# Optimization experiments

Measured on AMD Instinct MI355X. Metric: run time of the kernel, lower is better.

The kernel has to match this reference:

```python
import jax, jax.numpy as jnp
import numpy as np
from jax import lax

S, B, I, H, L = 512, 64, 256, 1024, 2

def setup_inputs() -> dict:
    key = jax.random.key(0)
    ks = jax.random.split(key, 9)
    s = 1.0 / np.sqrt(H)
    return {
        "x": jax.random.normal(ks[0], (S, B, I), jnp.float32),
        "W_in": jax.random.normal(ks[1], (H, I), jnp.float32) * (1.0 / np.sqrt(I)),
        "b_in": jax.random.normal(ks[2], (H,), jnp.float32) * 0.01,
        "W_ih": jax.random.normal(ks[3], (L, H, H), jnp.float32) * s,
        "W_hh": jax.random.normal(ks[4], (L, H, H), jnp.float32) * s,
        "b_ih": jax.random.normal(ks[5], (L, H), jnp.float32) * 0.01,
        "b_hh": jax.random.normal(ks[6], (L, H), jnp.float32) * 0.01,
        "W_out": jax.random.normal(ks[7], (I, H), jnp.float32) * s,
        "b_out": jax.random.normal(ks[8], (I,), jnp.float32) * 0.01,
    }

def reference(x, W_in, b_in, W_ih, W_hh, b_ih, b_hh, W_out, b_out):
    # in_layer: [S,B,I] -> [S,B,H]
    inp = jnp.einsum('sbi,hi->sbh', x, W_in) + b_in
    h0 = jnp.zeros((B, H), dtype=x.dtype)  # hidden=None -> zeros
    h_finals = []
    for l in range(L):  # fixed small layer loop
        # input-to-hidden GEMM batched over all timesteps
        pre = jnp.einsum('sbh,gh->sbg', inp, W_ih[l]) + b_ih[l]  # [S,B,H]
        Whh_l, bhh_l = W_hh[l], b_hh[l]
        def step(h, p, Whh=Whh_l, bhh=bhh_l):
            h_new = jnp.tanh(p + h @ Whh.T + bhh)
            return h_new, h_new
        h_last, inp = lax.scan(step, h0, pre)
        h_finals.append(h_last)
    hidden = jnp.stack(h_finals)  # [L,B,H]
    output = jnp.einsum('sbh,ih->sbi', inp, W_out) + b_out  # [S,B,I]
    return output, hidden
```

## Files before the change

kernel.cpp:

```cpp
#include <hip/hip_runtime.h>
#include <stdint.h>

#define SEQ 512
#define BAT 64
#define INF 256
#define HID 1024
#define SB  (SEQ*BAT)
#define G_WGS 64
#define NWG (3*G_WGS)

typedef __attribute__((ext_vector_type(8))) short short8;
typedef __attribute__((ext_vector_type(4))) float f32x4;

union Frag8 { uint32_t u[4]; short8 s; };

__device__ __forceinline__ uint32_t bf16hi_rne(uint32_t u){
  return (u + 0x7FFFu + ((u >> 16) & 1u)) & 0xFFFF0000u;
}
__device__ __forceinline__ uint32_t pack_split(float v){
  uint32_t hi = bf16hi_rne(__float_as_uint(v));
  float r = v - __uint_as_float(hi);
  uint32_t lo = bf16hi_rne(__float_as_uint(r)) >> 16;
  return hi | lo;
}
__device__ __forceinline__ void unpack_pair(uint32_t u0, uint32_t u1,
                                            uint32_t& h, uint32_t& l){
  h = __builtin_amdgcn_perm(u1, u0, 0x07060302u);
  l = __builtin_amdgcn_perm(u1, u0, 0x05040100u);
}
__device__ __forceinline__ void gl16(const void* g, void* l){
  __builtin_amdgcn_global_load_lds(
      (const __attribute__((address_space(1))) void*)g,
      (__attribute__((address_space(3))) void*)l, 16, 0, 0);
}

__device__ __forceinline__ void astore32(uint32_t* p, uint32_t v){
  __hip_atomic_store(p, v, __ATOMIC_RELAXED, __HIP_MEMORY_SCOPE_AGENT);
}
__device__ __forceinline__ void waitflags32(const uint32_t* base, uint32_t tgt){
  const int lane = threadIdx.x & 63;
  unsigned spins = 0;
  for (;;){
    uint32_t v = (lane < 32)
        ? __hip_atomic_load(base + lane, __ATOMIC_RELAXED, __HIP_MEMORY_SCOPE_AGENT)
        : 0xFFFFFFFFu;
    if (__all(v >= tgt)) break;
    __builtin_amdgcn_s_sleep(1);
    if (++spins > (1u << 20)) break;
  }
}

__global__ __launch_bounds__(256) void wcomb_kernel(const float* __restrict__ A,
                                                    const float* __restrict__ B,
                                                    float* __restrict__ C){
  __shared__ float As[16][64];
  __shared__ float Bs[64][256];
  const int tid = threadIdx.x;
  const int g0 = blockIdx.x * 16;
  float acc[16];
#pragma unroll
  for (int g = 0; g < 16; ++g) acc[g] = 0.f;
  for (int h0 = 0; h0 < HID; h0 += 64){
    __syncthreads();
#pragma unroll
    for (int j = 0; j < 4; ++j){
      int c = j*256 + tid;
      As[c >> 6][c & 63] = A[(size_t)(g0 + (c >> 6))*HID + h0 + (c & 63)];
    }
#pragma unroll
    for (int j = 0; j < 64; ++j) Bs[j][tid] = B[(size_t)(h0 + j)*INF + tid];
    __syncthreads();
#pragma unroll
    for (int hh = 0; hh < 64; hh += 4){
      float b0 = Bs[hh][tid], b1 = Bs[hh+1][tid], b2 = Bs[hh+2][tid], b3 = Bs[hh+3][tid];
#pragma unroll
      for (int g = 0; g < 16; ++g){
        const float4 a = *(const float4*)&As[g][hh];
        acc[g] += a.x*b0 + a.y*b1 + a.z*b2 + a.w*b3;
      }
    }
  }
#pragma unroll
  for (int g = 0; g < 16; ++g) C[(size_t)(g0 + g)*INF + tid] = acc[g];
}

__global__ __launch_bounds__(256) void bcomb_kernel(const float* __restrict__ Wih0,
                                                    const float* __restrict__ bin,
                                                    const float* __restrict__ bih0,
                                                    float* __restrict__ bcomb){
  __shared__ float r[4];
  const int g = blockIdx.x, tid = threadIdx.x;
  float s = 0.f;
  for (int h = tid; h < HID; h += 256) s += Wih0[(size_t)g*HID + h] * bin[h];
  for (int o = 32; o > 0; o >>= 1) s += __shfl_down(s, o, 64);
  if ((tid & 63) == 0) r[tid >> 6] = s;
  __syncthreads();
  if (tid == 0) bcomb[g] = bih0[g] + r[0] + r[1] + r[2] + r[3];
}

__global__ void split_w(const float* __restrict__ in, uint16_t* __restrict__ hi,
                        uint16_t* __restrict__ lo, int n){
  int i = blockIdx.x*256 + threadIdx.x;
  if (i < n){
    float v = in[i];
    uint32_t h = bf16hi_rne(__float_as_uint(v));
    float r = v - __uint_as_float(h);
    hi[i] = (uint16_t)(h >> 16);
    lo[i] = (uint16_t)(bf16hi_rne(__float_as_uint(r)) >> 16);
  }
}

__global__ void pack_x(const float* __restrict__ in, uint32_t* __restrict__ out, int n){
  int i = blockIdx.x*256 + threadIdx.x;
  if (i < n) out[i] = pack_split(in[i]);
}

__global__ __launch_bounds__(256) void gemm_split(
    const uint32_t* __restrict__ A, const uint16_t* __restrict__ Whi,
    const uint16_t* __restrict__ Wlo, const float* __restrict__ bias,
    float* __restrict__ C, int N, int K)
{
  __shared__ uint32_t Al[128*32];
  __shared__ uint16_t Wh[128*32];
  __shared__ uint16_t Wl[128*32];
  const int tid  = threadIdx.x;
  const int lane = tid & 63;
  const int w    = tid >> 6;
  const int wm   = w >> 1, wn = w & 1;
  const int lr   = lane & 15, kg = lane >> 4;
  const int bm   = blockIdx.x, bn = blockIdx.y;

  const uint32_t* Ag  = A   + (size_t)bm*128*K;
  const uint16_t* Whg = Whi + (size_t)bn*128*K;
  const uint16_t* Wlg = Wlo + (size_t)bn*128*K;

  f32x4 acc[4][4];
#pragma unroll
  for (int i = 0; i < 4; ++i)
#pragma unroll
    for (int j = 0; j < 4; ++j) acc[i][j] = (f32x4){0.f,0.f,0.f,0.f};

  for (int ks = 0; ks < K; ks += 32){
    __syncthreads();
#pragma unroll
    for (int j = 0; j < 4; ++j){
      int c = j*256 + tid;
      int row = c >> 3, kc = c & 7;
      int kcs = kc ^ ((row & 3) << 1);
      gl16(Ag + (size_t)row*K + ks + kcs*4, (char*)Al + c*16);
    }
#pragma unroll
    for (int j = 0; j < 2; ++j){
      int c = j*256 + tid;
      int row = c >> 2, kc = c & 3;
      int kcs = kc ^ (row & 3);
      gl16(Whg + (size_t)row*K + ks + kcs*8, (char*)Wh + c*16);
      gl16(Wlg + (size_t)row*K + ks + kcs*8, (char*)Wl + c*16);
    }
    __syncthreads();

    short8 ah[4], al[4];
#pragma unroll
    for (int mt = 0; mt < 4; ++mt){
      int row = wm*64 + mt*16 + lr;
      int c2  = kg ^ (row & 3);
      const uint32_t* p = &Al[row*32 + c2*8];
      uint4 a0 = *(const uint4*)p;
      uint4 a1 = *(const uint4*)(p + 4);
      Frag8 fh, fl;
      unpack_pair(a0.x, a0.y, fh.u[0], fl.u[0]);
      unpack_pair(a0.z, a0.w, fh.u[1], fl.u[1]);
      unpack_pair(a1.x, a1.y, fh.u[2], fl.u[2]);
      unpack_pair(a1.z, a1.w, fh.u[3], fl.u[3]);
      ah[mt] = fh.s; al[mt] = fl.s;
    }
#pragma unroll
    for (int nt = 0; nt < 4; ++nt){
      int row = wn*64 + nt*16 + lr;
      int kc  = kg ^ (row & 3);
      short8 whf = *(const short8*)&Wh[row*32 + kc*8];
      short8 wlf = *(const short8*)&Wl[row*32 + kc*8];
#pragma unroll
      for (int mt = 0; mt < 4; ++mt){
        acc[mt][nt] = __builtin_amdgcn_mfma_f32_16x16x32_bf16(ah[mt], whf, acc[mt][nt], 0,0,0);
        acc[mt][nt] = __builtin_amdgcn_mfma_f32_16x16x32_bf16(al[mt], whf, acc[mt][nt], 0,0,0);
        acc[mt][nt] = __builtin_amdgcn_mfma_f32_16x16x32_bf16(ah[mt], wlf, acc[mt][nt], 0,0,0);
      }
    }
  }
#pragma unroll
  for (int nt = 0; nt < 4; ++nt){
    int col = bn*128 + wn*64 + nt*16 + lr;
    float bv = bias[col];
#pragma unroll
    for (int mt = 0; mt < 4; ++mt){
#pragma unroll
      for (int r = 0; r < 4; ++r){
        int rowg = bm*128 + wm*64 + mt*16 + kg*4 + r;
        C[(size_t)rowg*N + col] = acc[mt][nt][r] + bv;
      }
    }
  }
}

__global__ __launch_bounds__(256, 1) void rnn_persist(
    const float* __restrict__ pre0, uint32_t* __restrict__ h0seq,
    uint32_t* __restrict__ pre1, uint32_t* __restrict__ h1seq,
    const uint16_t* __restrict__ Whh0h, const uint16_t* __restrict__ Whh0l,
    const uint16_t* __restrict__ Wih1h, const uint16_t* __restrict__ Wih1l,
    const uint16_t* __restrict__ Whh1h, const uint16_t* __restrict__ Whh1l,
    const float* __restrict__ bhh0, const float* __restrict__ bih1,
    const float* __restrict__ bhh1,
    uint32_t* h0s, uint32_t* h1s,
    uint32_t* ctr, int T, int first)
{
  __shared__ short WhF[32768];
  __shared__ short WlF[32768];
  __shared__ uint32_t Stage[4][2048];
  const int tid  = threadIdx.x;
  const int lane = tid & 63;
  const int w    = tid >> 6;
  const int mt   = w & 1, kh = w >> 1;
  const int lr   = lane & 15, kg = lane >> 4;
  const int wg   = blockIdx.x;
  const int group = wg / G_WGS;
  const int sub  = wg % G_WGS;
  const int rh   = sub >> 5;
  const int ci   = sub & 31;
  const int col0 = ci * 32;

  uint32_t* fmy = ctr + (group*2 + rh)*64;
  uint32_t* f0  = ctr + (0*2 + rh)*64;
  uint32_t* f1  = ctr + (1*2 + rh)*64;
  uint32_t* f2  = ctr + (2*2 + rh)*64;

  const uint16_t* Whg = (group == 0) ? Whh0h : (group == 1) ? Wih1h : Whh1h;
  const uint16_t* Wlg = (group == 0) ? Whh0l : (group == 1) ? Wih1l : Whh1l;

#pragma unroll
  for (int it = 0; it < 16; ++it){
    int lin = it*256 + tid;
    int c = lin >> 7, j = lin & 127;
    int dst = (((c >> 4)*32 + (j >> 2))*64 + (j & 3)*16 + (c & 15))*8;
    *(uint4*)&WhF[dst] = *(const uint4*)&Whg[(size_t)(col0 + c)*HID + j*8];
    *(uint4*)&WlF[dst] = *(const uint4*)&Wlg[(size_t)(col0 + c)*HID + j*8];
  }
  __syncthreads();

  const int p3r = ((lr & 3) << 1) | ((lr >> 2) & 1);
  const int fb0 = 0*16384 + lane*8;
  const int fb1 = 1*16384 + lane*8;
  const int colE = col0 + kh*16 + lr;
  float bvE = 0.f;
  if (group == 0) bvE = bhh0[colE];
  else if (group == 1) bvE = bih1[colE] + bhh1[colE];

  const int R = T + 2;
  for (int r = 0; r < R; ++r){
    const int t = r - group;
    const bool valid = (t >= 0 && t < T);

    if (valid){
      if (group == 0){
        if (t > 0) waitflags32(f0, (uint32_t)t);
      } else if (group == 1){
        waitflags32(f0, (uint32_t)(t+1));
      } else {
        waitflags32(f1, (uint32_t)(t+1));
        if (t > 0) waitflags32(f2, (uint32_t)t);
      }
      asm volatile("" ::: "memory");

      const uint32_t* Ap;
      if (group == 0)
        Ap = (t == 0) ? (first ? (const uint32_t*)0 : h0s)
                      : h0seq + (size_t)(t-1)*(BAT*HID);
      else if (group == 1)
        Ap = h0seq + (size_t)t*(BAT*HID);
      else
        Ap = (t == 0) ? (first ? (const uint32_t*)0 : h1s)
                      : h1seq + (size_t)(t-1)*(BAT*HID);

      const int rowb = rh*32 + mt*16 + kg*4;
      const size_t idxE = (size_t)t*(BAT*HID) + (size_t)rowb*HID + colE;
      float pv[4] = {0,0,0,0};
      if (group == 0){
#pragma unroll
        for (int q = 0; q < 4; ++q) pv[q] = pre0[idxE + (size_t)q*HID];
      } else if (group == 2){
#pragma unroll
        for (int q = 0; q < 4; ++q) pv[q] = __uint_as_float(pre1[idxE + (size_t)q*HID]);
      }

      f32x4 acc[2][2];
#pragma unroll
      for (int i = 0; i < 2; ++i)
#pragma unroll
        for (int j = 0; j < 2; ++j) acc[i][j] = (f32x4){0.f,0.f,0.f,0.f};

      if (Ap){
        const uint32_t* Aw = Ap + (size_t)(rh*32 + mt*16)*HID + kh*512;
        auto STAGE = [&](int c){
          char* dstbase = (char*)&Stage[w][(c & 1)*1024];
#pragma unroll
          for (int j = 0; j < 4; ++j){
            const int slot  = j*64 + lane;
            const int row_l = slot >> 4;
            const int pos   = slot & 15;
            const int p3 = ((row_l & 3) << 1) | ((row_l >> 2) & 1);
            gl16(Aw + (size_t)row_l*HID + c*64 + (pos ^ p3)*4,
                 dstbase + j*1024 + lane*16);
          }
        };

        STAGE(0);
#pragma unroll
        for (int c = 0; c < 8; ++c){
          if (c < 7){
            STAGE(c+1);
            asm volatile("s_waitcnt vmcnt(4)" ::: "memory");
          } else {
            asm volatile("s_waitcnt vmcnt(0)" ::: "memory");
          }
          const uint32_t* Ab = &Stage[w][(c & 1)*1024 + lr*64];
#pragma unroll
          for (int ksl = 0; ksl < 2; ++ksl){
            const int p0 = (ksl*8 + kg*2) ^ p3r;
            uint4 a0 = *(const uint4*)&Ab[p0*4];
            uint4 a1 = *(const uint4*)&Ab[(p0^1)*4];
            Frag8 fh, fl;
            unpack_pair(a0.x, a0.y, fh.u[0], fl.u[0]);
            unpack_pair(a0.z, a0.w, fh.u[1], fl.u[1]);
            unpack_pair(a1.x, a1.y, fh.u[2], fl.u[2]);
            unpack_pair(a1.z, a1.w, fh.u[3], fl.u[3]);
            const int ks = kh*16 + c*2 + ksl;
            short8 wh0 = *(const short8*)&WhF[fb0 + ks*512];
            short8 wl0 = *(const short8*)&WlF[fb0 + ks*512];
            short8 wh1 = *(const short8*)&WhF[fb1 + ks*512];
            short8 wl1 = *(const short8*)&WlF[fb1 + ks*512];
            acc[0][ksl] = __builtin_amdgcn_mfma_f32_16x16x32_bf16(fh.s, wh0, acc[0][ksl], 0,0,0);
            acc[0][ksl] = __builtin_amdgcn_mfma_f32_16x16x32_bf16(fl.s, wh0, acc[0][ksl], 0,0,0);
            acc[0][ksl] = __builtin_amdgcn_mfma_f32_16x16x32_bf16(fh.s, wl0, acc[0][ksl], 0,0,0);
            acc[1][ksl] = __builtin_amdgcn_mfma_f32_16x16x32_bf16(fh.s, wh1, acc[1][ksl], 0,0,0);
            acc[1][ksl] = __builtin_amdgcn_mfma_f32_16x16x32_bf16(fl.s, wh1, acc[1][ksl], 0,0,0);
            acc[1][ksl] = __builtin_amdgcn_mfma_f32_16x16x32_bf16(fh.s, wl1, acc[1][ksl], 0,0,0);
          }
        }
      }
      f32x4 sA = acc[0][0] + acc[0][1];
      f32x4 sB = acc[1][0] + acc[1][1];

      {
        f32x4 give = (kh == 0) ? sB : sA;
        *(f32x4*)&Stage[w][lane*8] = give;
        asm volatile("s_waitcnt lgkmcnt(0)" ::: "memory");
      }
      __builtin_amdgcn_s_barrier();
      {
        const int pw = w ^ 2;
        f32x4 part = *(const f32x4*)&Stage[pw][lane*8];
        f32x4 sE = (kh == 0) ? (sA + part) : (part + sB);

        if (group == 0){
#pragma unroll
          for (int q = 0; q < 4; ++q){
            float v = tanhf(sE[q] + pv[q] + bvE);
            uint32_t pk = pack_split(v);
            astore32(h0seq + idxE + (size_t)q*HID, pk);
            if (t == T-1) astore32(h0s + (size_t)(rowb + q)*HID + colE, pk);
          }
        } else if (group == 1){
#pragma unroll
          for (int q = 0; q < 4; ++q)
            astore32(pre1 + idxE + (size_t)q*HID, __float_as_uint(sE[q] + bvE));
        } else {
#pragma unroll
          for (int q = 0; q < 4; ++q){
            float v = tanhf(sE[q] + pv[q]);
            uint32_t pk = pack_split(v);
            astore32(h1seq + idxE + (size_t)q*HID, pk);
            if (t == T-1) astore32(h1s + (size_t)(rowb + q)*HID + colE, pk);
          }
        }
        asm volatile("s_waitcnt vmcnt(0)" ::: "memory");
      }
      __builtin_amdgcn_s_barrier();
      if (tid == 0)
        astore32(fmy + ci, (uint32_t)(t + 1));
    }
  }
}

__global__ void extract_hidden(const uint32_t* __restrict__ h0s,
                               const uint32_t* __restrict__ h1s,
                               float* __restrict__ out){
  int i = blockIdx.x*256 + threadIdx.x;
  uint32_t p = (i >> 16) ? h1s[i & 65535] : h0s[i & 65535];
  out[(size_t)SB*INF + i] = __uint_as_float(p & 0xFFFF0000u) + __uint_as_float(p << 16);
}

extern "C" void kernel_launch(void* const* d_in, const int* in_sizes, int n_in,
                              void* d_out, int out_size, void* d_ws, size_t ws_size,
                              hipStream_t stream)
{
  const float* x    = (const float*)d_in[0];
  const float* W_in = (const float*)d_in[1];
  const float* b_in = (const float*)d_in[2];
  const float* W_ih = (const float*)d_in[3];
  const float* W_hh = (const float*)d_in[4];
  const float* b_ih = (const float*)d_in[5];
  const float* b_hh = (const float*)d_in[6];
  const float* W_out= (const float*)d_in[7];
  const float* b_out= (const float*)d_in[8];
  float* out = (float*)d_out;
  (void)in_sizes; (void)n_in; (void)out_size;

  const size_t fixedB = 16257024 + 16384;
  const size_t perT   = 1114112;
  int T = 512;
  while (T > 2 && fixedB + (size_t)T*perT + 65536 > ws_size) T >>= 1;
  const int nchunk = SEQ / T;

  char* ws = (char*)d_ws;
  size_t off = 0;
  auto alloc = [&](size_t bytes)->void*{
    void* p = ws + off; off += (bytes + 255) & ~(size_t)255; return p;
  };
  float*    pre0s  = (float*)   alloc((size_t)T*BAT*HID*4);
  uint32_t* h0seq  = (uint32_t*)alloc((size_t)T*BAT*HID*4);
  uint32_t* pre1s  = (uint32_t*)alloc((size_t)T*BAT*HID*4);
  uint32_t* h1seq  = (uint32_t*)alloc((size_t)T*BAT*HID*4);
  uint32_t* xp     = (uint32_t*)alloc((size_t)T*BAT*INF*4);
  float*    WcombF = (float*)   alloc((size_t)HID*INF*4);
  uint16_t* Wc_hi  = (uint16_t*)alloc((size_t)HID*INF*2);
  uint16_t* Wc_lo  = (uint16_t*)alloc((size_t)HID*INF*2);
  uint16_t* Wih1_hi= (uint16_t*)alloc((size_t)HID*HID*2);
  uint16_t* Wih1_lo= (uint16_t*)alloc((size_t)HID*HID*2);
  uint16_t* Whh0_hi= (uint16_t*)alloc((size_t)HID*HID*2);
  uint16_t* Whh0_lo= (uint16_t*)alloc((size_t)HID*HID*2);
  uint16_t* Whh1_hi= (uint16_t*)alloc((size_t)HID*HID*2);
  uint16_t* Whh1_lo= (uint16_t*)alloc((size_t)HID*HID*2);
  uint16_t* Wout_hi= (uint16_t*)alloc((size_t)INF*HID*2);
  uint16_t* Wout_lo= (uint16_t*)alloc((size_t)INF*HID*2);
  float*    bcomb  = (float*)   alloc((size_t)HID*4);
  uint32_t* h0s    = (uint32_t*)alloc((size_t)BAT*HID*4);
  uint32_t* h1s    = (uint32_t*)alloc((size_t)BAT*HID*4);
  uint32_t* ctr    = (uint32_t*)alloc(8192);

  wcomb_kernel<<<HID/16, 256, 0, stream>>>(W_ih, W_in, WcombF);
  bcomb_kernel<<<HID, 256, 0, stream>>>(W_ih, b_in, b_ih, bcomb);
  split_w<<<(HID*INF+255)/256, 256, 0, stream>>>(WcombF, Wc_hi, Wc_lo, HID*INF);
  split_w<<<(HID*HID+255)/256, 256, 0, stream>>>(W_ih + (size_t)HID*HID, Wih1_hi, Wih1_lo, HID*HID);
  split_w<<<(HID*HID+255)/256, 256, 0, stream>>>(W_hh, Whh0_hi, Whh0_lo, HID*HID);
  split_w<<<(HID*HID+255)/256, 256, 0, stream>>>(W_hh + (size_t)HID*HID, Whh1_hi, Whh1_lo, HID*HID);
  split_w<<<(INF*HID+255)/256, 256, 0, stream>>>(W_out, Wout_hi, Wout_lo, INF*HID);

  for (int c = 0; c < nchunk; ++c){
    const float* xc = x + (size_t)c*T*BAT*INF;
    pack_x<<<T*BAT*INF/256, 256, 0, stream>>>(xc, xp, T*BAT*INF);
    gemm_split<<<dim3(T*64/128, HID/128), 256, 0, stream>>>(xp, Wc_hi, Wc_lo, bcomb, pre0s, HID, INF);
    hipMemsetAsync(ctr, 0, 8192, stream);
    rnn_persist<<<NWG, 256, 0, stream>>>(
        pre0s, h0seq, pre1s, h1seq,
        Whh0_hi, Whh0_lo, Wih1_hi, Wih1_lo, Whh1_hi, Whh1_lo,
        b_hh, b_ih + HID, b_hh + HID, h0s, h1s, ctr, T, (c == 0) ? 1 : 0);
    gemm_split<<<dim3(T*64/128, INF/128), 256, 0, stream>>>(h1seq, Wout_hi, Wout_lo,
                                                            b_out, out + (size_t)c*T*BAT*INF, INF, HID);
  }
  extract_hidden<<<(2*BAT*HID)/256, 256, 0, stream>>>(h0s, h1s, out);
}
```

Measured before the change: 4.705 ms.

## Store activations as single bf16 instead of hi/lo split, halving traffic and MFMAs

Activations (x, h0/h1 sequences, final hidden states) are now stored as a single bf16 value packed two per word instead of a bf16 hi+lo pair per fp32. This removes the lo-activation MFMA pass in both the GEMMs and the persistent recurrent kernel, halves activation memory traffic, and deepens the staging pipeline in the recurrent loop to four buffers. It lowers the precision of activations, including the returned hidden states, which may exceed tolerance over 512 recurrent steps.

New measurement: 3.917 ms, median of 2. 1.2x faster.

```diff
diff --git a/kernel.cpp b/kernel.cpp
--- a/kernel.cpp
+++ b/kernel.cpp
@@ -12,21 +12,11 @@
 typedef __attribute__((ext_vector_type(8))) short short8;
 typedef __attribute__((ext_vector_type(4))) float f32x4;
 
-union Frag8 { uint32_t u[4]; short8 s; };
-
 __device__ __forceinline__ uint32_t bf16hi_rne(uint32_t u){
   return (u + 0x7FFFu + ((u >> 16) & 1u)) & 0xFFFF0000u;
 }
-__device__ __forceinline__ uint32_t pack_split(float v){
-  uint32_t hi = bf16hi_rne(__float_as_uint(v));
-  float r = v - __uint_as_float(hi);
-  uint32_t lo = bf16hi_rne(__float_as_uint(r)) >> 16;
-  return hi | lo;
-}
-__device__ __forceinline__ void unpack_pair(uint32_t u0, uint32_t u1,
-                                            uint32_t& h, uint32_t& l){
-  h = __builtin_amdgcn_perm(u1, u0, 0x07060302u);
-  l = __builtin_amdgcn_perm(u1, u0, 0x05040100u);
+__device__ __forceinline__ uint32_t bf16_of(float v){
+  return bf16hi_rne(__float_as_uint(v)) >> 16;
 }
 __device__ __forceinline__ void gl16(const void* g, void* l){
   __builtin_amdgcn_global_load_lds(
@@ -110,17 +100,21 @@
   }
 }
 
-__global__ void pack_x(const float* __restrict__ in, uint32_t* __restrict__ out, int n){
+__global__ void pack_xb(const float* __restrict__ in, uint32_t* __restrict__ out, int n2){
   int i = blockIdx.x*256 + threadIdx.x;
-  if (i < n) out[i] = pack_split(in[i]);
-}
-
-__global__ __launch_bounds__(256) void gemm_split(
+  if (i < n2){
+    uint32_t a = bf16_of(in[2*i]);
+    uint32_t b = bf16_of(in[2*i + 1]);
+    out[i] = a | (b << 16);
+  }
+}
+
+__global__ __launch_bounds__(256) void gemm_bf16(
     const uint32_t* __restrict__ A, const uint16_t* __restrict__ Whi,
     const uint16_t* __restrict__ Wlo, const float* __restrict__ bias,
     float* __restrict__ C, int N, int K)
 {
-  __shared__ uint32_t Al[128*32];
+  __shared__ uint32_t Al[128*16];
   __shared__ uint16_t Wh[128*32];
   __shared__ uint16_t Wl[128*32];
   const int tid  = threadIdx.x;
@@ -129,8 +123,9 @@
   const int wm   = w >> 1, wn = w & 1;
   const int lr   = lane & 15, kg = lane >> 4;
   const int bm   = blockIdx.x, bn = blockIdx.y;
-
-  const uint32_t* Ag  = A   + (size_t)bm*128*K;
+  const int K2   = K >> 1;
+
+  const uint32_t* Ag  = A   + (size_t)bm*128*K2;
   const uint16_t* Whg = Whi + (size_t)bn*128*K;
   const uint16_t* Wlg = Wlo + (size_t)bn*128*K;
 
@@ -143,11 +138,11 @@
   for (int ks = 0; ks < K; ks += 32){
     __syncthreads();
 #pragma unroll
-    for (int j = 0; j < 4; ++j){
-      int c = j*256 + tid;
-      int row = c >> 3, kc = c & 7;
-      int kcs = kc ^ ((row & 3) << 1);
-      gl16(Ag + (size_t)row*K + ks + kcs*4, (char*)Al + c*16);
+    for (int j = 0; j < 2; ++j){
+      int s = j*256 + tid;
+      int row = s >> 2, pos = s & 3;
+      int ps = pos ^ (row & 3);
+      gl16(Ag + (size_t)row*K2 + (ks >> 1) + ps*4, (char*)Al + j*4096 + tid*16);
     }
 #pragma unroll
     for (int j = 0; j < 2; ++j){
@@ -159,20 +154,12 @@
     }
     __syncthreads();
 
-    short8 ah[4], al[4];
+    short8 ah[4];
 #pragma unroll
     for (int mt = 0; mt < 4; ++mt){
       int row = wm*64 + mt*16 + lr;
-      int c2  = kg ^ (row & 3);
-      const uint32_t* p = &Al[row*32 + c2*8];
-      uint4 a0 = *(const uint4*)p;
-      uint4 a1 = *(const uint4*)(p + 4);
-      Frag8 fh, fl;
-      unpack_pair(a0.x, a0.y, fh.u[0], fl.u[0]);
-      unpack_pair(a0.z, a0.w, fh.u[1], fl.u[1]);
-      unpack_pair(a1.x, a1.y, fh.u[2], fl.u[2]);
-      unpack_pair(a1.z, a1.w, fh.u[3], fl.u[3]);
-      ah[mt] = fh.s; al[mt] = fl.s;
+      int ps  = kg ^ (row & 3);
+      ah[mt] = *(const short8*)&Al[row*16 + ps*4];
     }
 #pragma unroll
     for (int nt = 0; nt < 4; ++nt){
@@ -183,7 +170,6 @@
 #pragma unroll
       for (int mt = 0; mt < 4; ++mt){
         acc[mt][nt] = __builtin_amdgcn_mfma_f32_16x16x32_bf16(ah[mt], whf, acc[mt][nt], 0,0,0);
-        acc[mt][nt] = __builtin_amdgcn_mfma_f32_16x16x32_bf16(al[mt], whf, acc[mt][nt], 0,0,0);
         acc[mt][nt] = __builtin_amdgcn_mfma_f32_16x16x32_bf16(ah[mt], wlf, acc[mt][nt], 0,0,0);
       }
     }
@@ -228,6 +214,7 @@
   const int rh   = sub >> 5;
   const int ci   = sub & 31;
   const int col0 = ci * 32;
+  const int H2   = HID/2;
 
   uint32_t* fmy = ctr + (group*2 + rh)*64;
   uint32_t* f0  = ctr + (0*2 + rh)*64;
@@ -274,22 +261,22 @@
       const uint32_t* Ap;
       if (group == 0)
         Ap = (t == 0) ? (first ? (const uint32_t*)0 : h0s)
-                      : h0seq + (size_t)(t-1)*(BAT*HID);
+                      : h0seq + (size_t)(t-1)*(BAT*H2);
       else if (group == 1)
-        Ap = h0seq + (size_t)t*(BAT*HID);
+        Ap = h0seq + (size_t)t*(BAT*H2);
       else
         Ap = (t == 0) ? (first ? (const uint32_t*)0 : h1s)
-                      : h1seq + (size_t)(t-1)*(BAT*HID);
+                      : h1seq + (size_t)(t-1)*(BAT*H2);
 
       const int rowb = rh*32 + mt*16 + kg*4;
-      const size_t idxE = (size_t)t*(BAT*HID) + (size_t)rowb*HID + colE;
+      const size_t idxP = (size_t)t*(BAT*HID) + (size_t)rowb*HID + colE;
       float pv[4] = {0,0,0,0};
       if (group == 0){
 #pragma unroll
-        for (int q = 0; q < 4; ++q) pv[q] = pre0[idxE + (size_t)q*HID];
+        for (int q = 0; q < 4; ++q) pv[q] = pre0[idxP + (size_t)q*HID];
       } else if (group == 2){
 #pragma unroll
-        for (int q = 0; q < 4; ++q) pv[q] = __uint_as_float(pre1[idxE + (size_t)q*HID]);
+        for (int q = 0; q < 4; ++q) pv[q] = __uint_as_float(pre1[idxP + (size_t)q*HID]);
       }
 
       f32x4 acc[2][2];
@@ -299,51 +286,40 @@
         for (int j = 0; j < 2; ++j) acc[i][j] = (f32x4){0.f,0.f,0.f,0.f};
 
       if (Ap){
-        const uint32_t* Aw = Ap + (size_t)(rh*32 + mt*16)*HID + kh*512;
+        const uint32_t* Aw = Ap + (size_t)(rh*32 + mt*16)*H2 + kh*256;
         auto STAGE = [&](int c){
-          char* dstbase = (char*)&Stage[w][(c & 1)*1024];
-#pragma unroll
-          for (int j = 0; j < 4; ++j){
-            const int slot  = j*64 + lane;
-            const int row_l = slot >> 4;
-            const int pos   = slot & 15;
-            const int p3 = ((row_l & 3) << 1) | ((row_l >> 2) & 1);
-            gl16(Aw + (size_t)row_l*HID + c*64 + (pos ^ p3)*4,
-                 dstbase + j*1024 + lane*16);
+          char* db = (char*)&Stage[w][(c & 3)*512];
+#pragma unroll
+          for (int j = 0; j < 2; ++j){
+            const int s   = j*64 + lane;
+            const int row = s >> 3, pos = s & 7;
+            const int p3  = ((row & 3) << 1) | ((row >> 2) & 1);
+            gl16(Aw + (size_t)row*H2 + c*32 + (pos ^ p3)*4, db + j*1024 + lane*16);
           }
         };
 
-        STAGE(0);
+        STAGE(0); STAGE(1); STAGE(2);
 #pragma unroll
         for (int c = 0; c < 8; ++c){
-          if (c < 7){
-            STAGE(c+1);
-            asm volatile("s_waitcnt vmcnt(4)" ::: "memory");
-          } else {
-            asm volatile("s_waitcnt vmcnt(0)" ::: "memory");
-          }
-          const uint32_t* Ab = &Stage[w][(c & 1)*1024 + lr*64];
-#pragma unroll
-          for (int ksl = 0; ksl < 2; ++ksl){
-            const int p0 = (ksl*8 + kg*2) ^ p3r;
-            uint4 a0 = *(const uint4*)&Ab[p0*4];
-            uint4 a1 = *(const uint4*)&Ab[(p0^1)*4];
-            Frag8 fh, fl;
-            unpack_pair(a0.x, a0.y, fh.u[0], fl.u[0]);
-            unpack_pair(a0.z, a0.w, fh.u[1], fl.u[1]);
-            unpack_pair(a1.x, a1.y, fh.u[2], fl.u[2]);
-            unpack_pair(a1.z, a1.w, fh.u[3], fl.u[3]);
-            const int ks = kh*16 + c*2 + ksl;
+          if (c < 5){
+            STAGE(c+3);
+            asm volatile("s_waitcnt vmcnt(6)" ::: "memory");
+          } else if (c == 5) asm volatile("s_waitcnt vmcnt(4)" ::: "memory");
+          else if (c == 6)   asm volatile("s_waitcnt vmcnt(2)" ::: "memory");
+          else               asm volatile("s_waitcnt vmcnt(0)" ::: "memory");
+          const char* Ab = (const char*)&Stage[w][(c & 3)*512] + lr*128;
+#pragma unroll
+          for (int j = 0; j < 2; ++j){
+            short8 af = *(const short8*)(Ab + ((((j << 2) | kg) ^ p3r)*16));
+            const int ks = kh*16 + c*2 + j;
             short8 wh0 = *(const short8*)&WhF[fb0 + ks*512];
             short8 wl0 = *(const short8*)&WlF[fb0 + ks*512];
             short8 wh1 = *(const short8*)&WhF[fb1 + ks*512];
             short8 wl1 = *(const short8*)&WlF[fb1 + ks*512];
-            acc[0][ksl] = __builtin_amdgcn_mfma_f32_16x16x32_bf16(fh.s, wh0, acc[0][ksl], 0,0,0);
-            acc[0][ksl] = __builtin_amdgcn_mfma_f32_16x16x32_bf16(fl.s, wh0, acc[0][ksl], 0,0,0);
-            acc[0][ksl] = __builtin_amdgcn_mfma_f32_16x16x32_bf16(fh.s, wl0, acc[0][ksl], 0,0,0);
-            acc[1][ksl] = __builtin_amdgcn_mfma_f32_16x16x32_bf16(fh.s, wh1, acc[1][ksl], 0,0,0);
-            acc[1][ksl] = __builtin_amdgcn_mfma_f32_16x16x32_bf16(fl.s, wh1, acc[1][ksl], 0,0,0);
-            acc[1][ksl] = __builtin_amdgcn_mfma_f32_16x16x32_bf16(fh.s, wl1, acc[1][ksl], 0,0,0);
+            acc[0][c & 1] = __builtin_amdgcn_mfma_f32_16x16x32_bf16(af, wh0, acc[0][c & 1], 0,0,0);
+            acc[0][c & 1] = __builtin_amdgcn_mfma_f32_16x16x32_bf16(af, wl0, acc[0][c & 1], 0,0,0);
+            acc[1][c & 1] = __builtin_amdgcn_mfma_f32_16x16x32_bf16(af, wh1, acc[1][c & 1], 0,0,0);
+            acc[1][c & 1] = __builtin_amdgcn_mfma_f32_16x16x32_bf16(af, wl1, acc[1][c & 1], 0,0,0);
           }
         }
       }
@@ -361,25 +337,24 @@
         f32x4 part = *(const f32x4*)&Stage[pw][lane*8];
         f32x4 sE = (kh == 0) ? (sA + part) : (part + sB);
 
-        if (group == 0){
+        if (group == 1){
+#pragma unroll
+          for (int q = 0; q < 4; ++q)
+            astore32(pre1 + idxP + (size_t)q*HID, __float_as_uint(sE[q] + bvE));
+        } else {
+          uint32_t* hseq = (group == 0) ? h0seq : h1seq;
+          uint32_t* hst  = (group == 0) ? h0s   : h1s;
+          const size_t idxH = (size_t)t*(BAT*H2) + (size_t)rowb*H2 + (colE >> 1);
 #pragma unroll
           for (int q = 0; q < 4; ++q){
-            float v = tanhf(sE[q] + pv[q] + bvE);
-            uint32_t pk = pack_split(v);
-            astore32(h0seq + idxE + (size_t)q*HID, pk);
-            if (t == T-1) astore32(h0s + (size_t)(rowb + q)*HID + colE, pk);
-          }
-        } else if (group == 1){
-#pragma unroll
-          for (int q = 0; q < 4; ++q)
-            astore32(pre1 + idxE + (size_t)q*HID, __float_as_uint(sE[q] + bvE));
-        } else {
-#pragma unroll
-          for (int q = 0; q < 4; ++q){
-            float v = tanhf(sE[q] + pv[q]);
-            uint32_t pk = pack_split(v);
-            astore32(h1seq + idxE + (size_t)q*HID, pk);
-            if (t == T-1) astore32(h1s + (size_t)(rowb + q)*HID + colE, pk);
+            float v = tanhf(sE[q] + pv[q] + ((group == 0) ? bvE : 0.f));
+            uint32_t b = bf16_of(v);
+            uint32_t o = (uint32_t)__shfl_xor((int)b, 1, 64);
+            if (!(lr & 1)){
+              uint32_t word = b | (o << 16);
+              astore32(hseq + idxH + (size_t)q*H2, word);
+              if (t == T-1) astore32(hst + (size_t)(rowb + q)*H2 + (colE >> 1), word);
+            }
           }
         }
         asm volatile("s_waitcnt vmcnt(0)" ::: "memory");
@@ -395,8 +370,11 @@
                                const uint32_t* __restrict__ h1s,
                                float* __restrict__ out){
   int i = blockIdx.x*256 + threadIdx.x;
-  uint32_t p = (i >> 16) ? h1s[i & 65535] : h0s[i & 65535];
-  out[(size_t)SB*INF + i] = __uint_as_float(p & 0xFFFF0000u) + __uint_as_float(p << 16);
+  int j = i & 65535;
+  const uint32_t* hs = (i >> 16) ? h1s : h0s;
+  uint32_t wv = hs[j >> 1];
+  uint32_t half = (j & 1) ? (wv >> 16) : (wv & 0xFFFFu);
+  out[(size_t)SB*INF + i] = __uint_as_float(half << 16);
 }
 
 extern "C" void kernel_launch(void* const* d_in, const int* in_sizes, int n_in,
@@ -415,10 +393,10 @@
   float* out = (float*)d_out;
   (void)in_sizes; (void)n_in; (void)out_size;
 
-  const size_t fixedB = 16257024 + 16384;
-  const size_t perT   = 1114112;
+  const size_t fixedB = 16500000;
+  const size_t perT   = 819200;
   int T = 512;
-  while (T > 2 && fixedB + (size_t)T*perT + 65536 > ws_size) T >>= 1;
+  while (T > 2 && fixedB + (size_t)T*perT > ws_size) T >>= 1;
   const int nchunk = SEQ / T;
 
   char* ws = (char*)d_ws;
@@ -427,10 +405,10 @@
     void* p = ws + off; off += (bytes + 255) & ~(size_t)255; return p;
   };
   float*    pre0s  = (float*)   alloc((size_t)T*BAT*HID*4);
-  uint32_t* h0seq  = (uint32_t*)alloc((size_t)T*BAT*HID*4);
+  uint32_t* h0seq  = (uint32_t*)alloc((size_t)T*BAT*(HID/2)*4);
   uint32_t* pre1s  = (uint32_t*)alloc((size_t)T*BAT*HID*4);
-  uint32_t* h1seq  = (uint32_t*)alloc((size_t)T*BAT*HID*4);
-  uint32_t* xp     = (uint32_t*)alloc((size_t)T*BAT*INF*4);
+  uint32_t* h1seq  = (uint32_t*)alloc((size_t)T*BAT*(HID/2)*4);
+  uint32_t* xp     = (uint32_t*)alloc((size_t)T*BAT*(INF/2)*4);
   float*    WcombF = (float*)   alloc((size_t)HID*INF*4);
   uint16_t* Wc_hi  = (uint16_t*)alloc((size_t)HID*INF*2);
   uint16_t* Wc_lo  = (uint16_t*)alloc((size_t)HID*INF*2);
@@ -443,8 +421,8 @@
   uint16_t* Wout_hi= (uint16_t*)alloc((size_t)INF*HID*2);
   uint16_t* Wout_lo= (uint16_t*)alloc((size_t)INF*HID*2);
   float*    bcomb  = (float*)   alloc((size_t)HID*4);
-  uint32_t* h0s    = (uint32_t*)alloc((size_t)BAT*HID*4);
-  uint32_t* h1s    = (uint32_t*)alloc((size_t)BAT*HID*4);
+  uint32_t* h0s    = (uint32_t*)alloc((size_t)BAT*(HID/2)*4);
+  uint32_t* h1s    = (uint32_t*)alloc((size_t)BAT*(HID/2)*4);
   uint32_t* ctr    = (uint32_t*)alloc(8192);
 
   wcomb_kernel<<<HID/16, 256, 0, stream>>>(W_ih, W_in, WcombF);
@@ -457,15 +435,15 @@
 
   for (int c = 0; c < nchunk; ++c){
     const float* xc = x + (size_t)c*T*BAT*INF;
-    pack_x<<<T*BAT*INF/256, 256, 0, stream>>>(xc, xp, T*BAT*INF);
-    gemm_split<<<dim3(T*64/128, HID/128), 256, 0, stream>>>(xp, Wc_hi, Wc_lo, bcomb, pre0s, HID, INF);
+    pack_xb<<<T*BAT*(INF/2)/256, 256, 0, stream>>>(xc, xp, T*BAT*(INF/2));
+    gemm_bf16<<<dim3(T*64/128, HID/128), 256, 0, stream>>>(xp, Wc_hi, Wc_lo, bcomb, pre0s, HID, INF);
     hipMemsetAsync(ctr, 0, 8192, stream);
     rnn_persist<<<NWG, 256, 0, stream>>>(
         pre0s, h0seq, pre1s, h1seq,
         Whh0_hi, Whh0_lo, Wih1_hi, Wih1_lo, Whh1_hi, Whh1_lo,
         b_hh, b_ih + HID, b_hh + HID, h0s, h1s, ctr, T, (c == 0) ? 1 : 0);
-    gemm_split<<<dim3(T*64/128, INF/128), 256, 0, stream>>>(h1seq, Wout_hi, Wout_lo,
-                                                            b_out, out + (size_t)c*T*BAT*INF, INF, HID);
+    gemm_bf16<<<dim3(T*64/128, INF/128), 256, 0, stream>>>(h1seq, Wout_hi, Wout_lo,
+                                                           b_out, out + (size_t)c*T*BAT*INF, INF, HID);
   }
   extract_hidden<<<(2*BAT*HID)/256, 256, 0, stream>>>(h0s, h1s, out);
 }
```
